# Kernel tuning notes

Hardware: AMD Instinct MI355X
Metric: run time of the kernel (lower is better)

Reference implementation:

```python
import jax, jax.numpy as jnp
import numpy as np

EMB, HEADS, LAT, FFN = 1024, 16, 256, 4096
HD = EMB // HEADS
B, N = 2, 2048

def _ln(x, w, b, eps=1e-5):
    mu = jnp.mean(x, axis=-1, keepdims=True)
    var = jnp.var(x, axis=-1, keepdims=True)
    return (x - mu) * jax.lax.rsqrt(var + eps) * w + b

def setup_inputs() -> dict:
    key = jax.random.key(0)
    ks = jax.random.split(key, 16)
    def lin(k, fan_in, fan_out):
        bound = 1.0 / np.sqrt(fan_in)
        kw, kb = jax.random.split(k)
        W = jax.random.uniform(kw, (fan_in, fan_out), jnp.float32, -bound, bound)
        b = jax.random.uniform(kb, (fan_out,), jnp.float32, -bound, bound)
        return W, b
    Wq, bq = lin(ks[0], EMB, EMB)
    WaK, baK = lin(ks[1], EMB, LAT)
    WbK, bbK = lin(ks[2], LAT, EMB)
    WaV, baV = lin(ks[3], EMB, LAT)
    WbV, bbV = lin(ks[4], LAT, EMB)
    Wo, bo = lin(ks[5], EMB, EMB)
    W1, b1 = lin(ks[6], EMB, FFN)
    W2, b2 = lin(ks[7], FFN, EMB)
    return {
        'x': jax.random.normal(ks[8], (B, N, EMB), jnp.float32),
        'attn_bias': jax.random.normal(ks[9], (N, N), jnp.float32),
        'Wq': Wq, 'bq': bq, 'WaK': WaK, 'baK': baK, 'WbK': WbK, 'bbK': bbK,
        'WaV': WaV, 'baV': baV, 'WbV': WbV, 'bbV': bbV, 'Wo': Wo, 'bo': bo,
        'W1': W1, 'b1': b1, 'W2': W2, 'b2': b2,
        'ln1_w': jnp.ones((EMB,), jnp.float32), 'ln1_b': jnp.zeros((EMB,), jnp.float32),
        'ln2_w': jnp.ones((EMB,), jnp.float32), 'ln2_b': jnp.zeros((EMB,), jnp.float32),
    }

def reference(x, attn_bias, Wq, bq, WaK, baK, WbK, bbK, WaV, baV, WbV, bbV,
              Wo, bo, W1, b1, W2, b2, ln1_w, ln1_b, ln2_w, ln2_b):
    Q = x @ Wq + bq                       # [B,N,E]
    K = (x @ WaK + baK) @ WbK + bbK       # low-rank K
    V = (x @ WaV + baV) @ WbV + bbV       # low-rank V
    def split(t):
        return t.reshape(B, N, HEADS, HD).transpose(0, 2, 1, 3)  # [B,H,N,D]
    Qh, Kh, Vh = split(Q), split(K), split(V)
    scores = jnp.einsum('bhnd,bhmd->bhnm', Qh, Kh) / np.sqrt(HD)
    scores = scores + attn_bias[None, None]
    weights = jax.nn.softmax(scores, axis=-1)
    attn = jnp.einsum('bhnm,bhmd->bhnd', weights, Vh)
    attn = attn.transpose(0, 2, 1, 3).reshape(B, N, EMB)
    attn = attn @ Wo + bo
    h = _ln(x + attn, ln1_w, ln1_b)
    ffn = jax.nn.gelu(h @ W1 + b1, approximate=False) @ W2 + b2
    return _ln(h + ffn, ln2_w, ln2_b)
```

## Files before the change

kernel.cpp:

```cpp
#include <hip/hip_runtime.h>
#include <hip/hip_bf16.h>
#include <math.h>

typedef unsigned short u16;
typedef short bf16x8 __attribute__((ext_vector_type(8)));
typedef float f32x4 __attribute__((ext_vector_type(4)));

#define EMB   1024
#define HEADS 16
#define HD    64
#define LATD  256
#define FFND  4096
#define BATCH 2
#define SEQ   2048
#define TOK   (BATCH*SEQ)

__device__ __forceinline__ float bf2f(u16 u) {
    union { unsigned int i; float f; } x; x.i = ((unsigned int)u) << 16; return x.f;
}
__device__ __forceinline__ u16 f2bf(float f) {
    union { float f; unsigned int i; } x; x.f = f;
    unsigned int i = x.i;
    unsigned int lsb = (i >> 16) & 1u;
    i += 0x7fffu + lsb;
    return (u16)(i >> 16);
}
__device__ __forceinline__ void gld16(const u16* g, u16* l) {
    __builtin_amdgcn_global_load_lds(
        (const __attribute__((address_space(1))) void*)g,
        (__attribute__((address_space(3))) void*)l, 16, 0, 0);
}
__device__ __forceinline__ unsigned int cvt_pk_bf16(float a, float b) {
    unsigned int r;
    asm("v_cvt_pk_bf16_f32 %0, %1, %2" : "=v"(r) : "v"(a), "v"(b));
    return r;
}
#if defined(__has_builtin)
#if __has_builtin(__builtin_amdgcn_exp2f)
#define EXP2(x) __builtin_amdgcn_exp2f(x)
#endif
#endif
#ifndef EXP2
#define EXP2(x) exp2f(x)
#endif

__global__ __launch_bounds__(256) void cvt_f32_bf16_kernel(
    const float* __restrict__ in, u16* __restrict__ out, int n8)
{
    int i = blockIdx.x * 256 + threadIdx.x;
    int stride = gridDim.x * 256;
    for (; i < n8; i += stride) {
        float4 f0 = *(const float4*)(in + (size_t)i * 8);
        float4 f1 = *(const float4*)(in + (size_t)i * 8 + 4);
        u16 e[8];
        e[0] = f2bf(f0.x); e[1] = f2bf(f0.y); e[2] = f2bf(f0.z); e[3] = f2bf(f0.w);
        e[4] = f2bf(f1.x); e[5] = f2bf(f1.y); e[6] = f2bf(f1.z); e[7] = f2bf(f1.w);
        *(uint4*)(out + (size_t)i * 8) = *(const uint4*)e;
    }
}

__global__ __launch_bounds__(256) void concat_bias_kernel(
    const float* __restrict__ a, const float* __restrict__ b, float* __restrict__ out)
{
    int i = blockIdx.x * 256 + threadIdx.x;
    out[i] = (i < 256) ? a[i] : b[i - 256];
}

__global__ __launch_bounds__(256) void permute_ab_kernel(
    const float* __restrict__ ab, float* __restrict__ abP)
{
    const int kt = blockIdx.x, qt = blockIdx.y;
    const int tid = threadIdx.x;
    const int lane = tid & 63, wq = tid >> 6;
    const int qq = lane >> 4, col = lane & 15;
#pragma unroll
    for (int wi = wq; wi < 8; wi += 4)
#pragma unroll
        for (int mt = 0; mt < 4; mt++) {
            float4 v = *(const float4*)(ab + (size_t)(qt * 128 + wi * 16 + col) * SEQ
                                        + kt * 64 + mt * 16 + qq * 4);
            v.x *= 8.f; v.y *= 8.f; v.z *= 8.f; v.w *= 8.f;
            *(float4*)(abP + (((size_t)qt * 32 + kt) * 8 + wi) * 1024 + mt * 256 + lane * 4) = v;
        }
}

struct TDesc { const float* src; u16* dst; int K; int N; int ofs; };
struct TTable { TDesc d[8]; };

__global__ __launch_bounds__(256) void transpose_all_kernel(TTable tt)
{
    __shared__ u16 t[32][33];
    int tb = blockIdx.x, e = 0;
#pragma unroll
    for (int i = 1; i < 8; i++) if (tb >= tt.d[i].ofs) e = i;
    const float* src = tt.d[e].src;
    u16* dst = tt.d[e].dst;
    const int K = tt.d[e].K, N = tt.d[e].N;
    const int local = tb - tt.d[e].ofs;
    const int nx = N >> 5;
    const int bx = (local % nx) * 32;
    const int by = (local / nx) * 32;
    const int tx = threadIdx.x & 31;
    const int ty = threadIdx.x >> 5;
#pragma unroll
    for (int i = 0; i < 32; i += 8)
        t[ty + i][tx] = f2bf(src[(size_t)(by + ty + i) * N + bx + tx]);
    __syncthreads();
#pragma unroll
    for (int i = 0; i < 32; i += 8)
        dst[(size_t)(bx + ty + i) * K + by + tx] = t[tx][ty + i];
}

#define BM 128
#define GBK 64

template <int ACT, int BNv>
__device__ __forceinline__ void gemm_body(
    const u16* __restrict__ A, int lda, const u16* __restrict__ WT,
    const float* __restrict__ bias, u16* __restrict__ C,
    int K, int N, int bx, u16* Al, u16* Wl)
{
    const int NT = BNv / 32;
    const int WN = BNv / 2;
    const int CW = BNv / 32;

    const int tid  = threadIdx.x;
    const int lane = tid & 63;
    const int w    = tid >> 6;
    const int wm = w >> 1, wn = w & 1;
    const int col = lane & 15, qq = lane >> 4;
    const size_t bm = (size_t)blockIdx.y * BM;
    const size_t bn = (size_t)bx * BNv;

    f32x4 acc[4][NT];
#pragma unroll
    for (int mt = 0; mt < 4; mt++)
#pragma unroll
        for (int nt = 0; nt < NT; nt++) acc[mt][nt] = (f32x4){0.f, 0.f, 0.f, 0.f};

    const u16* gA[4]; u16* lA[4];
#pragma unroll
    for (int i = 0; i < 4; i++) {
        int f = w * 256 + i * 64 + lane;
        int r = f >> 3, s = f & 7, sg = s ^ (r & 7);
        gA[i] = A + (bm + r) * (size_t)lda + sg * 8;
        lA[i] = &Al[(size_t)(w * 256 + i * 64) * 8];
    }
    const u16* gW[4]; u16* lW[4];
#pragma unroll
    for (int i = 0; i < CW; i++) {
        int f = w * (BNv * 2) + i * 64 + lane;
        int r = f >> 3, s = f & 7, sg = s ^ (r & 7);
        gW[i] = WT + (bn + r) * (size_t)K + sg * 8;
        lW[i] = &Wl[(size_t)(w * (BNv * 2) + i * 64) * 8];
    }

    for (int k0 = 0; k0 < K; k0 += GBK) {
#pragma unroll
        for (int i = 0; i < 4; i++) gld16(gA[i] + k0, lA[i]);
#pragma unroll
        for (int i = 0; i < CW; i++) gld16(gW[i] + k0, lW[i]);
        __syncthreads();

#pragma unroll
        for (int kk = 0; kk < 2; kk++) {
            bf16x8 af[4], bfr[NT];
#pragma unroll
            for (int mt = 0; mt < 4; mt++) {
                int rr = wm * 64 + mt * 16 + col;
                int sub = (kk * 4 + qq) ^ (rr & 7);
                af[mt] = *(const bf16x8*)&Al[rr * GBK + sub * 8];
            }
#pragma unroll
            for (int nt = 0; nt < NT; nt++) {
                int rn = wn * WN + nt * 16 + col;
                int sub = (kk * 4 + qq) ^ (rn & 7);
                bfr[nt] = *(const bf16x8*)&Wl[rn * GBK + sub * 8];
            }
#pragma unroll
            for (int mt = 0; mt < 4; mt++)
#pragma unroll
                for (int nt = 0; nt < NT; nt++)
                    acc[mt][nt] = __builtin_amdgcn_mfma_f32_16x16x32_bf16(
                        af[mt], bfr[nt], acc[mt][nt], 0, 0, 0);
        }
        __syncthreads();
    }

    float bv[NT];
#pragma unroll
    for (int nt = 0; nt < NT; nt++)
        bv[nt] = bias[bn + wn * WN + nt * 16 + col];

#pragma unroll
    for (int mt = 0; mt < 4; mt++) {
#pragma unroll
        for (int nt = 0; nt < NT; nt++) {
#pragma unroll
            for (int r = 0; r < 4; r++) {
                float v = acc[mt][nt][r] + bv[nt];
                if (ACT == 1) v = 0.5f * v * (1.0f + erff(v * 0.70710678118654752f));
                size_t rg = bm + wm * 64 + mt * 16 + qq * 4 + r;
                C[rg * (size_t)N + bn + wn * WN + nt * 16 + col] = f2bf(v);
            }
        }
    }
}

template <int ACT, int BNv, int MINW>
__global__ __launch_bounds__(256, MINW) void gemm_bt_kernel(
    const u16* __restrict__ A, int lda, const u16* __restrict__ WT,
    const float* __restrict__ bias, u16* __restrict__ C,
    int K, int N)
{
    __shared__ __align__(16) u16 Al[BM * GBK];
    __shared__ __align__(16) u16 Wl[BNv * GBK];
    gemm_body<ACT, BNv>(A, lda, WT, bias, C, K, N, blockIdx.x, Al, Wl);
}

struct GPair {
    const u16* A0; const u16* A1;
    const u16* W0; const u16* W1;
    const float* b0; const float* b1;
    u16* C0; u16* C1;
    int lda0, lda1, N0, N1, nx0;
};

template <int BNv, int MINW>
__global__ __launch_bounds__(256, MINW) void gemm_pair_kernel(GPair p, int K)
{
    __shared__ __align__(16) u16 Al[BM * GBK];
    __shared__ __align__(16) u16 Wl[BNv * GBK];
    const bool s1 = (int)blockIdx.x >= p.nx0;
    const u16* A = s1 ? p.A1 : p.A0;
    const u16* WT = s1 ? p.W1 : p.W0;
    const float* bias = s1 ? p.b1 : p.b0;
    u16* C = s1 ? p.C1 : p.C0;
    const int lda = s1 ? p.lda1 : p.lda0;
    const int N = s1 ? p.N1 : p.N0;
    const int bx = s1 ? (int)blockIdx.x - p.nx0 : (int)blockIdx.x;
    gemm_body<0, BNv>(A, lda, WT, bias, C, K, N, bx, Al, Wl);
}

#define BQ   128
#define BKV  64
#define NKVT (SEQ / BKV)
#define LDK  72
#define LDP  72
#define LDV  72
#define SCL2 0.18033688011112042f

__global__ __launch_bounds__(512, 4) void fattn_kernel(
    const u16* __restrict__ Q, const u16* __restrict__ K,
    const u16* __restrict__ V, const float* __restrict__ abP,
    u16* __restrict__ O)
{
    __shared__ __align__(16) u16 Ks[BKV * LDK];
    __shared__ __align__(16) u16 Ps[BQ * LDP];
    __shared__ __align__(16) u16 Vt[HD * LDV];

    const int tid = threadIdx.x;
    const int lane = tid & 63;
    const int w = tid >> 6;
    const int col = lane & 15, qq = lane >> 4;
    const int qt = blockIdx.x;
    const int b = blockIdx.y >> 4, h = blockIdx.y & 15;
    const size_t tok0 = (size_t)b * SEQ + (size_t)qt * BQ;
    const int wrow = w * 16;
    const size_t kvbase = (size_t)b * SEQ * EMB + h * HD;

    const int krow = tid >> 3, kcol = (tid & 7) * 8;
    const int vrow = tid & 63, vdg = tid >> 6;

    bf16x8 aq[2];
#pragma unroll
    for (int kk = 0; kk < 2; kk++)
        aq[kk] = *(const bf16x8*)(Q + (tok0 + wrow + col) * EMB + h * HD + kk * 32 + qq * 8);

    float m_st = -1e30f, l_st = 0.f;
    f32x4 o_acc[4];
#pragma unroll
    for (int dt = 0; dt < 4; dt++) o_acc[dt] = (f32x4){0.f, 0.f, 0.f, 0.f};

    uint4 kreg, vreg;
#define LOADKV(KV0) do {                                                              \
        kreg = *(const uint4*)(K + kvbase + (size_t)((KV0) + krow) * EMB + kcol);     \
        vreg = *(const uint4*)(V + kvbase + (size_t)((KV0) + vrow) * EMB + vdg * 8);  \
    } while (0)

    LOADKV(0);

    for (int t = 0; t < NKVT; t++) {
        *(uint4*)&Ks[krow * LDK + kcol] = kreg;
        {
            u16 vv[8]; *(uint4*)vv = vreg;
#pragma unroll
            for (int dd = 0; dd < 8; dd++)
                Vt[(vdg * 8 + dd) * LDV + vrow] = vv[dd];
        }
        __syncthreads();

        if (t + 1 < NKVT) LOADKV((t + 1) * BKV);

        const float* abb = abP + (((size_t)qt * NKVT + t) * 8 + w) * 1024;
        f32x4 s2[4];
#pragma unroll
        for (int mt = 0; mt < 4; mt++)
            s2[mt] = *(const f32x4*)(abb + mt * 256 + lane * 4);
#pragma unroll
        for (int mt = 0; mt < 4; mt++) {
            bf16x8 ak0 = *(const bf16x8*)&Ks[(mt * 16 + col) * LDK + qq * 8];
            bf16x8 ak1 = *(const bf16x8*)&Ks[(mt * 16 + col) * LDK + 32 + qq * 8];
            s2[mt] = __builtin_amdgcn_mfma_f32_16x16x32_bf16(ak0, aq[0], s2[mt], 0, 0, 0);
            s2[mt] = __builtin_amdgcn_mfma_f32_16x16x32_bf16(ak1, aq[1], s2[mt], 0, 0, 0);
        }
#pragma unroll
        for (int mt = 0; mt < 4; mt++)
#pragma unroll
            for (int r = 0; r < 4; r++) s2[mt][r] *= SCL2;

        float t0 = fmaxf(fmaxf(s2[0][0], s2[0][1]), fmaxf(s2[0][2], s2[0][3]));
        float t1 = fmaxf(fmaxf(s2[1][0], s2[1][1]), fmaxf(s2[1][2], s2[1][3]));
        float t2 = fmaxf(fmaxf(s2[2][0], s2[2][1]), fmaxf(s2[2][2], s2[2][3]));
        float t3 = fmaxf(fmaxf(s2[3][0], s2[3][1]), fmaxf(s2[3][2], s2[3][3]));
        float tm = fmaxf(fmaxf(t0, t1), fmaxf(t2, t3));
        tm = fmaxf(tm, __shfl_xor(tm, 16));
        tm = fmaxf(tm, __shfl_xor(tm, 32));
        float mnew = fmaxf(m_st, tm);
        float alpha = EXP2(m_st - mnew);
        m_st = mnew;
        float rs = 0.f;
#pragma unroll
        for (int mt = 0; mt < 4; mt++)
#pragma unroll
            for (int r = 0; r < 4; r++) {
                float e = EXP2(s2[mt][r] - mnew);
                s2[mt][r] = e;
                rs += e;
            }
        rs += __shfl_xor(rs, 16);
        rs += __shfl_xor(rs, 32);
        l_st = l_st * alpha + rs;

        float af[4];
#pragma unroll
        for (int r = 0; r < 4; r++) af[r] = __shfl(alpha, qq * 20 + r);
#pragma unroll
        for (int dt = 0; dt < 4; dt++)
#pragma unroll
            for (int r = 0; r < 4; r++) o_acc[dt][r] *= af[r];

#pragma unroll
        for (int mt = 0; mt < 4; mt++) {
            uint2 pp;
            pp.x = cvt_pk_bf16(s2[mt][0], s2[mt][1]);
            pp.y = cvt_pk_bf16(s2[mt][2], s2[mt][3]);
            *(uint2*)&Ps[(wrow + col) * LDP + mt * 16 + qq * 4] = pp;
        }

#pragma unroll
        for (int kk = 0; kk < 2; kk++) {
            bf16x8 ap = *(const bf16x8*)&Ps[(wrow + col) * LDP + kk * 32 + qq * 8];
#pragma unroll
            for (int dt = 0; dt < 4; dt++) {
                bf16x8 bv = *(const bf16x8*)&Vt[(dt * 16 + col) * LDV + kk * 32 + qq * 8];
                o_acc[dt] = __builtin_amdgcn_mfma_f32_16x16x32_bf16(ap, bv, o_acc[dt], 0, 0, 0);
            }
        }
        __syncthreads();
    }
#undef LOADKV

    float lr[4];
#pragma unroll
    for (int r = 0; r < 4; r++) lr[r] = 1.0f / __shfl(l_st, qq * 20 + r);
#pragma unroll
    for (int r = 0; r < 4; r++)
#pragma unroll
        for (int dt = 0; dt < 4; dt++)
            O[(tok0 + wrow + qq * 4 + r) * EMB + h * HD + dt * 16 + col]
                = f2bf(o_acc[dt][r] * lr[r]);
}

template <int AF32, int OUTF32>
__global__ __launch_bounds__(256) void ln_kernel(
    const void* __restrict__ A, const u16* __restrict__ R,
    const float* __restrict__ w, const float* __restrict__ bb,
    void* __restrict__ out)
{
    __shared__ float r1[4], r2[4];
    const int tid = threadIdx.x;
    const size_t row = blockIdx.x;

    float v[4];
    float s = 0.0f, s2 = 0.0f;
#pragma unroll
    for (int i = 0; i < 4; i++) {
        int c = tid + i * 256;
        float a = AF32 ? ((const float*)A)[row * EMB + c]
                       : bf2f(((const u16*)A)[row * EMB + c]);
        float t = a + bf2f(R[row * EMB + c]);
        v[i] = t;
        s += t; s2 += t * t;
    }
#pragma unroll
    for (int o = 32; o > 0; o >>= 1) {
        s  += __shfl_down(s, o);
        s2 += __shfl_down(s2, o);
    }
    if ((tid & 63) == 0) { r1[tid >> 6] = s; r2[tid >> 6] = s2; }
    __syncthreads();
    s  = r1[0] + r1[1] + r1[2] + r1[3];
    s2 = r2[0] + r2[1] + r2[2] + r2[3];

    float mu = s * (1.0f / EMB);
    float var = s2 * (1.0f / EMB) - mu * mu;
    float rs = rsqrtf(var + 1e-5f);

#pragma unroll
    for (int i = 0; i < 4; i++) {
        int c = tid + i * 256;
        float y = (v[i] - mu) * rs * w[c] + bb[c];
        if (OUTF32) ((float*)out)[row * EMB + c] = y;
        else        ((u16*)out)[row * EMB + c] = f2bf(y);
    }
}

extern "C" void kernel_launch(void* const* d_in, const int* in_sizes, int n_in,
                              void* d_out, int out_size, void* d_ws, size_t ws_size,
                              hipStream_t stream)
{
    const float* x    = (const float*)d_in[0];
    const float* ab   = (const float*)d_in[1];
    const float* Wq   = (const float*)d_in[2];
    const float* bq   = (const float*)d_in[3];
    const float* WaK  = (const float*)d_in[4];
    const float* baK  = (const float*)d_in[5];
    const float* WbK  = (const float*)d_in[6];
    const float* bbK  = (const float*)d_in[7];
    const float* WaV  = (const float*)d_in[8];
    const float* baV  = (const float*)d_in[9];
    const float* WbV  = (const float*)d_in[10];
    const float* bbV  = (const float*)d_in[11];
    const float* Wo   = (const float*)d_in[12];
    const float* bo   = (const float*)d_in[13];
    const float* W1   = (const float*)d_in[14];
    const float* b1   = (const float*)d_in[15];
    const float* W2   = (const float*)d_in[16];
    const float* b2   = (const float*)d_in[17];
    const float* ln1w = (const float*)d_in[18];
    const float* ln1b = (const float*)d_in[19];
    const float* ln2w = (const float*)d_in[20];
    const float* ln2b = (const float*)d_in[21];

    u16* w = (u16*)d_ws;
    size_t o = 0;
    u16* WqT  = w + o; o += (size_t)EMB * EMB;
    u16* WaKT = w + o; o += (size_t)EMB * LATD;
    u16* WaVT = w + o; o += (size_t)EMB * LATD;
    u16* WbKT = w + o; o += (size_t)LATD * EMB;
    u16* WbVT = w + o; o += (size_t)LATD * EMB;
    u16* WoT  = w + o; o += (size_t)EMB * EMB;
    u16* W1T  = w + o; o += (size_t)EMB * FFND;
    u16* W2T  = w + o; o += (size_t)FFND * EMB;
    u16* Qb   = w + o; o += (size_t)TOK * EMB;
    u16* Kb   = w + o; o += (size_t)TOK * EMB;
    u16* Vb   = w + o; o += (size_t)TOK * EMB;
    u16* aOb  = w + o; o += (size_t)TOK * EMB;
    u16* projb= w + o; o += (size_t)TOK * EMB;
    u16* hb   = w + o; o += (size_t)TOK * EMB;
    u16* xb   = w + o; o += (size_t)TOK * EMB;
    float* bKV = (float*)(w + o); o += 1024;
    float* abP = (float*)projb;
    u16* KVa = aOb;
    u16* f1  = Qb;
    u16* f2  = projb;

    dim3 blk(256);

    cvt_f32_bf16_kernel<<<dim3(2048), blk, 0, stream>>>(x, xb, TOK * EMB / 8);
    concat_bias_kernel<<<dim3(2), blk, 0, stream>>>(baK, baV, bKV);
    permute_ab_kernel<<<dim3(32, 16), blk, 0, stream>>>(ab, abP);

    TTable tt;
    tt.d[0] = {Wq,  WqT,  EMB,  EMB,  0};
    tt.d[1] = {WaK, WaKT, EMB,  LATD, 1024};
    tt.d[2] = {WaV, WaVT, EMB,  LATD, 1280};
    tt.d[3] = {WbK, WbKT, LATD, EMB,  1536};
    tt.d[4] = {WbV, WbVT, LATD, EMB,  1792};
    tt.d[5] = {Wo,  WoT,  EMB,  EMB,  2048};
    tt.d[6] = {W1,  W1T,  EMB,  FFND, 3072};
    tt.d[7] = {W2,  W2T,  FFND, EMB,  7168};
    transpose_all_kernel<<<dim3(11264), blk, 0, stream>>>(tt);

    {
        GPair p;
        p.A0 = xb;  p.A1 = xb;
        p.W0 = WqT; p.W1 = WaKT;
        p.b0 = bq;  p.b1 = bKV;
        p.C0 = Qb;  p.C1 = KVa;
        p.lda0 = EMB; p.lda1 = EMB;
        p.N0 = EMB; p.N1 = 512; p.nx0 = 16;
        gemm_pair_kernel<64, 3><<<dim3(24, TOK / BM), blk, 0, stream>>>(p, EMB);
    }
    {
        GPair p;
        p.A0 = KVa;  p.A1 = KVa + LATD;
        p.W0 = WbKT; p.W1 = WbVT;
        p.b0 = bbK;  p.b1 = bbV;
        p.C0 = Kb;   p.C1 = Vb;
        p.lda0 = 512; p.lda1 = 512;
        p.N0 = EMB; p.N1 = EMB; p.nx0 = 16;
        gemm_pair_kernel<64, 3><<<dim3(32, TOK / BM), blk, 0, stream>>>(p, LATD);
    }

    fattn_kernel<<<dim3(SEQ / BQ, BATCH * HEADS), dim3(512), 0, stream>>>(Qb, Kb, Vb, abP, aOb);

    gemm_bt_kernel<0,64,3><<<dim3(EMB / 64, TOK / BM), blk, 0, stream>>>(aOb, EMB, WoT, bo, projb, EMB, EMB);

    ln_kernel<1,0><<<dim3(TOK), blk, 0, stream>>>(x, projb, ln1w, ln1b, hb);

    gemm_bt_kernel<1,128,2><<<dim3(FFND / 128, TOK / BM), blk, 0, stream>>>(hb, EMB, W1T, b1, f1, EMB, FFND);
    gemm_bt_kernel<0,64,3><<<dim3(EMB / 64, TOK / BM), blk, 0, stream>>>(f1, FFND, W2T, b2, f2, FFND, EMB);

    ln_kernel<0,1><<<dim3(TOK), blk, 0, stream>>>(hb, f2, ln2w, ln2b, (float*)d_out);
}
```

Measured before the change: 389.1 us.

## Double-buffer K/V in flash attention, fold softmax scale into Wq, lazy rescale

The attention kernel now double-buffers the K and V tiles in shared memory, cutting one barrier per iteration, and prefetches the bias tile one iteration ahead. The 1/sqrt(d)*log2e scale is folded into Wq and bq during the weight transpose, and the bias is premultiplied by log2e, which removes the per-score multiply. The running-max rescale of the output accumulator is skipped unless the new max exceeds the old one by more than 8, and s_setprio is raised around the MFMA blocks. The cost is more LDS per block, which may reduce occupancy, more live registers, and rounding Wq to bf16 after scaling, which changes numerics slightly.

```diff
diff --git a/kernel.cpp b/kernel.cpp
--- a/kernel.cpp
+++ b/kernel.cpp
@@ -14,6 +14,9 @@
 #define BATCH 2
 #define SEQ   2048
 #define TOK   (BATCH*SEQ)
+
+#define SCL2  0.18033688011112042f
+#define LOG2E 1.4426950408889634f
 
 __device__ __forceinline__ float bf2f(u16 u) {
     union { unsigned int i; float f; } x; x.i = ((unsigned int)u) << 16; return x.f;
@@ -59,11 +62,14 @@
     }
 }
 
-__global__ __launch_bounds__(256) void concat_bias_kernel(
-    const float* __restrict__ a, const float* __restrict__ b, float* __restrict__ out)
+__global__ __launch_bounds__(256) void prep_bias_kernel(
+    const float* __restrict__ a, const float* __restrict__ b,
+    const float* __restrict__ q, float* __restrict__ bKV, float* __restrict__ bqs)
 {
     int i = blockIdx.x * 256 + threadIdx.x;
-    out[i] = (i < 256) ? a[i] : b[i - 256];
+    if (i < 256)      bKV[i] = a[i];
+    else if (i < 512) bKV[i] = b[i - 256];
+    else              bqs[i - 512] = q[i - 512] * SCL2;
 }
 
 __global__ __launch_bounds__(256) void permute_ab_kernel(
@@ -79,12 +85,12 @@
         for (int mt = 0; mt < 4; mt++) {
             float4 v = *(const float4*)(ab + (size_t)(qt * 128 + wi * 16 + col) * SEQ
                                         + kt * 64 + mt * 16 + qq * 4);
-            v.x *= 8.f; v.y *= 8.f; v.z *= 8.f; v.w *= 8.f;
+            v.x *= LOG2E; v.y *= LOG2E; v.z *= LOG2E; v.w *= LOG2E;
             *(float4*)(abP + (((size_t)qt * 32 + kt) * 8 + wi) * 1024 + mt * 256 + lane * 4) = v;
         }
 }
 
-struct TDesc { const float* src; u16* dst; int K; int N; int ofs; };
+struct TDesc { const float* src; u16* dst; int K; int N; int ofs; float scl; };
 struct TTable { TDesc d[8]; };
 
 __global__ __launch_bounds__(256) void transpose_all_kernel(TTable tt)
@@ -96,6 +102,7 @@
     const float* src = tt.d[e].src;
     u16* dst = tt.d[e].dst;
     const int K = tt.d[e].K, N = tt.d[e].N;
+    const float scl = tt.d[e].scl;
     const int local = tb - tt.d[e].ofs;
     const int nx = N >> 5;
     const int bx = (local % nx) * 32;
@@ -104,7 +111,7 @@
     const int ty = threadIdx.x >> 5;
 #pragma unroll
     for (int i = 0; i < 32; i += 8)
-        t[ty + i][tx] = f2bf(src[(size_t)(by + ty + i) * N + bx + tx]);
+        t[ty + i][tx] = f2bf(src[(size_t)(by + ty + i) * N + bx + tx] * scl);
     __syncthreads();
 #pragma unroll
     for (int i = 0; i < 32; i += 8)
@@ -248,16 +255,15 @@
 #define LDK  72
 #define LDP  72
 #define LDV  72
-#define SCL2 0.18033688011112042f
 
 __global__ __launch_bounds__(512, 4) void fattn_kernel(
     const u16* __restrict__ Q, const u16* __restrict__ K,
     const u16* __restrict__ V, const float* __restrict__ abP,
     u16* __restrict__ O)
 {
-    __shared__ __align__(16) u16 Ks[BKV * LDK];
+    __shared__ __align__(16) u16 Ks[2][BKV * LDK];
+    __shared__ __align__(16) u16 Vt[2][HD * LDV];
     __shared__ __align__(16) u16 Ps[BQ * LDP];
-    __shared__ __align__(16) u16 Vt[HD * LDV];
 
     const int tid = threadIdx.x;
     const int lane = tid & 63;
@@ -289,35 +295,54 @@
     } while (0)
 
     LOADKV(0);
+    *(uint4*)&Ks[0][krow * LDK + kcol] = kreg;
+    {
+        u16 vv[8]; *(uint4*)vv = vreg;
+#pragma unroll
+        for (int dd = 0; dd < 8; dd++)
+            Vt[0][(vdg * 8 + dd) * LDV + vrow] = vv[dd];
+    }
+    __syncthreads();
+    LOADKV(BKV);
+
+    const float* abq = abP + (size_t)qt * NKVT * 8192 + (size_t)w * 1024;
+    f32x4 abv[4];
+#pragma unroll
+    for (int mt = 0; mt < 4; mt++)
+        abv[mt] = *(const f32x4*)(abq + mt * 256 + lane * 4);
 
     for (int t = 0; t < NKVT; t++) {
-        *(uint4*)&Ks[krow * LDK + kcol] = kreg;
-        {
-            u16 vv[8]; *(uint4*)vv = vreg;
-#pragma unroll
-            for (int dd = 0; dd < 8; dd++)
-                Vt[(vdg * 8 + dd) * LDV + vrow] = vv[dd];
-        }
-        __syncthreads();
-
-        if (t + 1 < NKVT) LOADKV((t + 1) * BKV);
-
-        const float* abb = abP + (((size_t)qt * NKVT + t) * 8 + w) * 1024;
+        const int cur = t & 1;
+        const u16* Kc = Ks[cur];
+
         f32x4 s2[4];
 #pragma unroll
-        for (int mt = 0; mt < 4; mt++)
-            s2[mt] = *(const f32x4*)(abb + mt * 256 + lane * 4);
+        for (int mt = 0; mt < 4; mt++) s2[mt] = abv[mt];
+        __builtin_amdgcn_s_setprio(1);
 #pragma unroll
         for (int mt = 0; mt < 4; mt++) {
-            bf16x8 ak0 = *(const bf16x8*)&Ks[(mt * 16 + col) * LDK + qq * 8];
-            bf16x8 ak1 = *(const bf16x8*)&Ks[(mt * 16 + col) * LDK + 32 + qq * 8];
+            bf16x8 ak0 = *(const bf16x8*)&Kc[(mt * 16 + col) * LDK + qq * 8];
+            bf16x8 ak1 = *(const bf16x8*)&Kc[(mt * 16 + col) * LDK + 32 + qq * 8];
             s2[mt] = __builtin_amdgcn_mfma_f32_16x16x32_bf16(ak0, aq[0], s2[mt], 0, 0, 0);
             s2[mt] = __builtin_amdgcn_mfma_f32_16x16x32_bf16(ak1, aq[1], s2[mt], 0, 0, 0);
         }
-#pragma unroll
-        for (int mt = 0; mt < 4; mt++)
-#pragma unroll
-            for (int r = 0; r < 4; r++) s2[mt][r] *= SCL2;
+        __builtin_amdgcn_s_setprio(0);
+
+        if (t + 1 < NKVT) {
+            const float* abn = abq + (size_t)(t + 1) * 8192;
+#pragma unroll
+            for (int mt = 0; mt < 4; mt++)
+                abv[mt] = *(const f32x4*)(abn + mt * 256 + lane * 4);
+        }
+
+        if (t + 1 < NKVT) {
+            *(uint4*)&Ks[cur ^ 1][krow * LDK + kcol] = kreg;
+            u16 vv[8]; *(uint4*)vv = vreg;
+#pragma unroll
+            for (int dd = 0; dd < 8; dd++)
+                Vt[cur ^ 1][(vdg * 8 + dd) * LDV + vrow] = vv[dd];
+        }
+        if (t + 2 < NKVT) LOADKV((t + 2) * BKV);
 
         float t0 = fmaxf(fmaxf(s2[0][0], s2[0][1]), fmaxf(s2[0][2], s2[0][3]));
         float t1 = fmaxf(fmaxf(s2[1][0], s2[1][1]), fmaxf(s2[1][2], s2[1][3]));
@@ -326,29 +351,31 @@
         float tm = fmaxf(fmaxf(t0, t1), fmaxf(t2, t3));
         tm = fmaxf(tm, __shfl_xor(tm, 16));
         tm = fmaxf(tm, __shfl_xor(tm, 32));
-        float mnew = fmaxf(m_st, tm);
-        float alpha = EXP2(m_st - mnew);
-        m_st = mnew;
+        if (!__all(tm <= m_st + 8.f)) {
+            float mnew = fmaxf(m_st, tm);
+            float alpha = EXP2(m_st - mnew);
+            m_st = mnew;
+            l_st *= alpha;
+            float af[4];
+#pragma unroll
+            for (int r = 0; r < 4; r++) af[r] = __shfl(alpha, qq * 20 + r);
+#pragma unroll
+            for (int dt = 0; dt < 4; dt++)
+#pragma unroll
+                for (int r = 0; r < 4; r++) o_acc[dt][r] *= af[r];
+        }
         float rs = 0.f;
 #pragma unroll
         for (int mt = 0; mt < 4; mt++)
 #pragma unroll
             for (int r = 0; r < 4; r++) {
-                float e = EXP2(s2[mt][r] - mnew);
+                float e = EXP2(s2[mt][r] - m_st);
                 s2[mt][r] = e;
                 rs += e;
             }
         rs += __shfl_xor(rs, 16);
         rs += __shfl_xor(rs, 32);
-        l_st = l_st * alpha + rs;
-
-        float af[4];
-#pragma unroll
-        for (int r = 0; r < 4; r++) af[r] = __shfl(alpha, qq * 20 + r);
-#pragma unroll
-        for (int dt = 0; dt < 4; dt++)
-#pragma unroll
-            for (int r = 0; r < 4; r++) o_acc[dt][r] *= af[r];
+        l_st += rs;
 
 #pragma unroll
         for (int mt = 0; mt < 4; mt++) {
@@ -358,15 +385,17 @@
             *(uint2*)&Ps[(wrow + col) * LDP + mt * 16 + qq * 4] = pp;
         }
 
+        __builtin_amdgcn_s_setprio(1);
 #pragma unroll
         for (int kk = 0; kk < 2; kk++) {
             bf16x8 ap = *(const bf16x8*)&Ps[(wrow + col) * LDP + kk * 32 + qq * 8];
 #pragma unroll
             for (int dt = 0; dt < 4; dt++) {
-                bf16x8 bv = *(const bf16x8*)&Vt[(dt * 16 + col) * LDV + kk * 32 + qq * 8];
+                bf16x8 bv = *(const bf16x8*)&Vt[cur][(dt * 16 + col) * LDV + kk * 32 + qq * 8];
                 o_acc[dt] = __builtin_amdgcn_mfma_f32_16x16x32_bf16(ap, bv, o_acc[dt], 0, 0, 0);
             }
         }
+        __builtin_amdgcn_s_setprio(0);
         __syncthreads();
     }
 #undef LOADKV
@@ -471,6 +500,7 @@
     u16* hb   = w + o; o += (size_t)TOK * EMB;
     u16* xb   = w + o; o += (size_t)TOK * EMB;
     float* bKV = (float*)(w + o); o += 1024;
+    float* bqs = (float*)(w + o); o += 2048;
     float* abP = (float*)projb;
     u16* KVa = aOb;
     u16* f1  = Qb;
@@ -479,25 +509,25 @@
     dim3 blk(256);
 
     cvt_f32_bf16_kernel<<<dim3(2048), blk, 0, stream>>>(x, xb, TOK * EMB / 8);
-    concat_bias_kernel<<<dim3(2), blk, 0, stream>>>(baK, baV, bKV);
+    prep_bias_kernel<<<dim3(6), blk, 0, stream>>>(baK, baV, bq, bKV, bqs);
     permute_ab_kernel<<<dim3(32, 16), blk, 0, stream>>>(ab, abP);
 
     TTable tt;
-    tt.d[0] = {Wq,  WqT,  EMB,  EMB,  0};
-    tt.d[1] = {WaK, WaKT, EMB,  LATD, 1024};
-    tt.d[2] = {WaV, WaVT, EMB,  LATD, 1280};
-    tt.d[3] = {WbK, WbKT, LATD, EMB,  1536};
-    tt.d[4] = {WbV, WbVT, LATD, EMB,  1792};
-    tt.d[5] = {Wo,  WoT,  EMB,  EMB,  2048};
-    tt.d[6] = {W1,  W1T,  EMB,  FFND, 3072};
-    tt.d[7] = {W2,  W2T,  FFND, EMB,  7168};
+    tt.d[0] = {Wq,  WqT,  EMB,  EMB,  0,    SCL2};
+    tt.d[1] = {WaK, WaKT, EMB,  LATD, 1024, 1.0f};
+    tt.d[2] = {WaV, WaVT, EMB,  LATD, 1280, 1.0f};
+    tt.d[3] = {WbK, WbKT, LATD, EMB,  1536, 1.0f};
+    tt.d[4] = {WbV, WbVT, LATD, EMB,  1792, 1.0f};
+    tt.d[5] = {Wo,  WoT,  EMB,  EMB,  2048, 1.0f};
+    tt.d[6] = {W1,  W1T,  EMB,  FFND, 3072, 1.0f};
+    tt.d[7] = {W2,  W2T,  FFND, EMB,  7168, 1.0f};
     transpose_all_kernel<<<dim3(11264), blk, 0, stream>>>(tt);
 
     {
         GPair p;
         p.A0 = xb;  p.A1 = xb;
         p.W0 = WqT; p.W1 = WaKT;
-        p.b0 = bq;  p.b1 = bKV;
+        p.b0 = bqs; p.b1 = bKV;
         p.C0 = Qb;  p.C1 = KVa;
         p.lda0 = EMB; p.lda1 = EMB;
         p.N0 = EMB; p.N1 = 512; p.nx0 = 16;
```

Measured after the change: 389.7 us. About the same (+0.1%).
